# Kernel optimization log

Measured on AMD Instinct MI355X. Metric: run time of the kernel, lower is better.

## Reference

```python
import jax, jax.numpy as jnp
import numpy as np

DT = 0.01
NJ = 7
GRAV = 9.81
Q_LOWER = jnp.array([-2.9671, -1.8326, -2.9671, -3.1416, -2.9671, -0.0873, -2.9671], jnp.float32)
Q_UPPER = jnp.array([ 2.9671,  1.8326,  2.9671,  0.0,     2.9671,  3.8223,  2.9671], jnp.float32)


def _skew(v):
    z = jnp.zeros((), v.dtype)
    return jnp.stack([jnp.stack([z, -v[2], v[1]]),
                      jnp.stack([v[2], z, -v[0]]),
                      jnp.stack([-v[1], v[0], z])])


def _mot_X(E, r):
    # 6x6 spatial motion transform [[E,0],[-E*skew(r),E]]
    zero = jnp.zeros_like(E)
    top = jnp.concatenate([E, zero], axis=1)
    bot = jnp.concatenate([-E @ _skew(r), E], axis=1)
    return jnp.concatenate([top, bot], axis=0)


def _crm(v):
    # spatial motion cross-product matrix for v=[w;v0]
    Sw, Sv = _skew(v[:3]), _skew(v[3:])
    zero = jnp.zeros_like(Sw)
    top = jnp.concatenate([Sw, zero], axis=1)
    bot = jnp.concatenate([Sv, Sw], axis=1)
    return jnp.concatenate([top, bot], axis=0)


def _step_single(x, u, axes, R_tree, p_tree, I_sp):
    dt_ = x.dtype
    q = jnp.clip(x[:NJ], Q_LOWER.astype(dt_), Q_UPPER.astype(dt_))
    qd = x[NJ:]
    # forward kinematics: per-joint 6x6 child<-parent transforms and motion subspaces
    Xups, Ss = [], []
    eye3 = jnp.eye(3, dtype=dt_)
    for i in range(NJ):
        a = axes[i]
        c, s = jnp.cos(q[i]), jnp.sin(q[i])
        R = c * eye3 + s * _skew(a) + (1.0 - c) * jnp.outer(a, a)  # rodrigues
        Xj = _mot_X(R.T, jnp.zeros(3, dt_))
        Xt = _mot_X(R_tree[i], p_tree[i])
        Xups.append(Xj @ Xt)
        Ss.append(jnp.concatenate([a, jnp.zeros(3, dt_)]))
    # RNEA bias force h (qdd=0, gravity, zero base velocity, identity base pose)
    v_prev = jnp.zeros(6, dt_)
    a_prev = jnp.array([0.0, 0.0, 0.0, 0.0, 0.0, GRAV], dt_)  # a_base = -g trick
    fs = []
    for i in range(NJ):
        vJ = Ss[i] * qd[i]
        v = Xups[i] @ v_prev + vJ
        acc = Xups[i] @ a_prev + _crm(v) @ vJ
        Iv = I_sp[i] @ v
        f = I_sp[i] @ acc - _crm(v).T @ Iv  # crf(v) = -crm(v)^T
        fs.append(f)
        v_prev, a_prev = v, acc
    h = [None] * NJ
    for i in range(NJ - 1, -1, -1):
        h[i] = Ss[i] @ fs[i]
        if i > 0:
            fs[i - 1] = fs[i - 1] + Xups[i].T @ fs[i]
    h = jnp.stack(h)
    # CRBA mass matrix (serial chain, parent(i)=i-1)
    Ic = [I_sp[i] for i in range(NJ)]
    M = jnp.zeros((NJ, NJ), dt_)
    for i in range(NJ - 1, -1, -1):
        if i > 0:
            Ic[i - 1] = Ic[i - 1] + Xups[i].T @ Ic[i] @ Xups[i]
        F = Ic[i] @ Ss[i]
        M = M.at[i, i].set(Ss[i] @ F)
        for j in range(i - 1, -1, -1):
            F = Xups[j + 1].T @ F
            mij = Ss[j] @ F
            M = M.at[i, j].set(mij).at[j, i].set(mij)
    M = M + 1e-8 * jnp.eye(NJ, dtype=dt_)
    qdd = jnp.linalg.solve(M, (u - h)[:, None])[:, 0]
    qd_new = qd + DT * qdd
    q_new = q + DT * qd_new
    return jnp.concatenate([q_new, qd_new])


def setup_inputs() -> dict:
    B = 65536
    key = jax.random.key(0)
    k1, k2 = jax.random.split(key)
    x = jax.random.normal(k1, (B, 14), jnp.float32)
    u = jax.random.normal(k2, (B, 7), jnp.float32)
    rng = np.random.default_rng(0)
    # unit joint axes
    axes = rng.normal(size=(NJ, 3))
    axes = axes / np.linalg.norm(axes, axis=1, keepdims=True)
    # orthonormal fixed parent->child rotations (det +1)
    R_tree = np.empty((NJ, 3, 3))
    for i in range(NJ):
        Q, _ = np.linalg.qr(rng.normal(size=(3, 3)))
        if np.linalg.det(Q) < 0:
            Q[:, 0] = -Q[:, 0]
        R_tree[i] = Q
    p_tree = 0.2 * rng.normal(size=(NJ, 3))
    # SPD 6x6 spatial inertias: [[Ibar, m*Cx],[m*Cx^T, m*I3]]
    I_sp = np.empty((NJ, 6, 6))
    for i in range(NJ):
        m = float(rng.uniform(1.0, 5.0))
        c = 0.05 * rng.normal(size=3)
        Cx = np.array([[0, -c[2], c[1]], [c[2], 0, -c[0]], [-c[1], c[0], 0]])
        A = 0.1 * rng.normal(size=(3, 3))
        Ic_ = A @ A.T + 0.05 * np.eye(3)
        Ibar = Ic_ + m * Cx @ Cx.T
        I_sp[i] = np.block([[Ibar, m * Cx], [m * Cx.T, m * np.eye(3)]])
    return {
        "x": x, "u": u,
        "axes": jnp.asarray(axes, jnp.float32),
        "R_tree": jnp.asarray(R_tree, jnp.float32),
        "p_tree": jnp.asarray(p_tree, jnp.float32),
        "I_sp": jnp.asarray(I_sp, jnp.float32),
    }


def reference(x, u, axes, R_tree, p_tree, I_sp):
    return jax.vmap(_step_single, in_axes=(0, 0, None, None, None, None))(
        x, u, axes, R_tree, p_tree, I_sp)
```

## Files before the change

### kernel.cpp

```cpp
#include <hip/hip_runtime.h>
#include <math.h>

#define NJ 7
#define DTF 0.01f
#define GRAVF 9.81f
#define MIX(i,j) ((i)*((i)+1)/2 + (j))
#define MPAD 29

__device__ __forceinline__ void cross3(const float* a, const float* b, float* o){
    o[0] = a[1]*b[2] - a[2]*b[1];
    o[1] = a[2]*b[0] - a[0]*b[2];
    o[2] = a[0]*b[1] - a[1]*b[0];
}
__device__ __forceinline__ void mtv3(const float* E, const float* x, float* y){
    y[0] = E[0]*x[0] + E[3]*x[1] + E[6]*x[2];
    y[1] = E[1]*x[0] + E[4]*x[1] + E[7]*x[2];
    y[2] = E[2]*x[0] + E[5]*x[1] + E[8]*x[2];
}
__device__ __forceinline__ void symv(const float* S, const float* x, float* y){
    y[0] = S[0]*x[0] + S[1]*x[1] + S[2]*x[2];
    y[1] = S[1]*x[0] + S[3]*x[1] + S[4]*x[2];
    y[2] = S[2]*x[0] + S[4]*x[1] + S[5]*x[2];
}
__device__ __forceinline__ void mm3(const float* A, const float* B, float* o){
#pragma unroll
    for (int r = 0; r < 3; r++)
#pragma unroll
        for (int c = 0; c < 3; c++)
            o[r*3+c] = A[r*3]*B[c] + A[r*3+1]*B[3+c] + A[r*3+2]*B[6+c];
}
__device__ __forceinline__ void congr(const float* E, const float* X, float* o){
    float t[9];
#pragma unroll
    for (int r = 0; r < 3; r++)
#pragma unroll
        for (int c = 0; c < 3; c++)
            t[r*3+c] = E[r]*X[c] + E[3+r]*X[3+c] + E[6+r]*X[6+c];
    mm3(t, E, o);
}
__device__ __forceinline__ void makeE(const float* a, const float* __restrict__ Rt,
                                      float s, float c, float* E){
    float omc = 1.0f - c;
    float RT[9];
    RT[0] = c + omc*a[0]*a[0];       RT[1] =  s*a[2] + omc*a[0]*a[1]; RT[2] = -s*a[1] + omc*a[0]*a[2];
    RT[3] = -s*a[2] + omc*a[1]*a[0]; RT[4] = c + omc*a[1]*a[1];       RT[5] =  s*a[0] + omc*a[1]*a[2];
    RT[6] =  s*a[1] + omc*a[2]*a[0]; RT[7] = -s*a[0] + omc*a[2]*a[1]; RT[8] = c + omc*a[2]*a[2];
    float Rl[9];
#pragma unroll
    for (int k = 0; k < 9; k++) Rl[k] = Rt[k];
    mm3(RT, Rl, E);
}
__device__ __forceinline__ void bodyI(const float* __restrict__ g_I, int i,
                                      float* SA, float* h, float& m){
    const float* I6 = g_I + i*36;
    SA[0]=I6[0]; SA[1]=I6[1]; SA[2]=I6[2];
    SA[3]=I6[7]; SA[4]=I6[8]; SA[5]=I6[14];
    h[0]=I6[16]; h[1]=I6[5]; h[2]=I6[9];
    m = I6[21];
}
__device__ __forceinline__ void congrBase(const float* Ec, const float* rc,
                                          const float* SA, const float* h, float m,
                                          float* SA0, float* h0){
    float Af[9] = {SA[0],SA[1],SA[2], SA[1],SA[3],SA[4], SA[2],SA[4],SA[5]};
    float Ap[9]; congr(Ec, Af, Ap);
    float hr[3]; mtv3(Ec, h, hr);
    float hpd = hr[0]*rc[0]+hr[1]*rc[1]+hr[2]*rc[2];
    float ppd = rc[0]*rc[0]+rc[1]*rc[1]+rc[2]*rc[2];
    float dga = 2.0f*hpd + m*ppd;
    SA0[0] = Ap[0] - 2.0f*rc[0]*hr[0] - m*rc[0]*rc[0] + dga;
    SA0[1] = Ap[1] - rc[0]*hr[1] - hr[0]*rc[1] - m*rc[0]*rc[1];
    SA0[2] = Ap[2] - rc[0]*hr[2] - hr[0]*rc[2] - m*rc[0]*rc[2];
    SA0[3] = Ap[4] - 2.0f*rc[1]*hr[1] - m*rc[1]*rc[1] + dga;
    SA0[4] = Ap[5] - rc[1]*hr[2] - hr[1]*rc[2] - m*rc[1]*rc[2];
    SA0[5] = Ap[8] - 2.0f*rc[2]*hr[2] - m*rc[2]*rc[2] + dga;
    h0[0] = hr[0] + m*rc[0];
    h0[1] = hr[1] + m*rc[1];
    h0[2] = hr[2] + m*rc[2];
}

__constant__ float QL_c[NJ] = {-2.9671f,-1.8326f,-2.9671f,-3.1416f,-2.9671f,-0.0873f,-2.9671f};
__constant__ float QU_c[NJ] = { 2.9671f, 1.8326f, 2.9671f, 0.0f,    2.9671f, 3.8223f, 2.9671f};

__global__ __launch_bounds__(128)
void panda_step(const float* __restrict__ x, const float* __restrict__ u,
                const float* __restrict__ g_ax, const float* __restrict__ g_Rt,
                const float* __restrict__ g_pt, const float* __restrict__ g_I,
                float* __restrict__ out, int B)
{
    __shared__ float s_M[64*MPAD];

    const int role = threadIdx.x >> 6;
    const int lane = threadIdx.x & 63;
    const int e    = blockIdx.x*64 + lane;
    const bool act = (e < B);

    float q[NJ], qd[NJ], sn[NJ], cs[NJ];
    if (act){
        float xl[14];
        const float2* x2 = (const float2*)(x + e*14);
#pragma unroll
        for (int i = 0; i < 7; i++){ float2 v = x2[i]; xl[2*i] = v.x; xl[2*i+1] = v.y; }
#pragma unroll
        for (int i = 0; i < NJ; i++){
            q[i]  = fminf(fmaxf(xl[i], QL_c[i]), QU_c[i]);
            qd[i] = xl[NJ + i];
            __sincosf(q[i], &sn[i], &cs[i]);
        }
    }

    float rhs[NJ];

    if (act && role == 1){
        float Sw[NJ][3], Sv[NJ][3];
        float SB[NJ][6], hB[NJ][3];
        float Ec[9], rc[3];
#pragma unroll
        for (int i = 0; i < NJ; i++){
            float a[3] = { g_ax[3*i], g_ax[3*i+1], g_ax[3*i+2] };
            float p[3] = { g_pt[3*i], g_pt[3*i+1], g_pt[3*i+2] };
            float E[9]; makeE(a, g_Rt + 9*i, sn[i], cs[i], E);
            if (i == 0){
#pragma unroll
                for (int k = 0; k < 9; k++) Ec[k] = E[k];
                rc[0]=p[0]; rc[1]=p[1]; rc[2]=p[2];
            } else {
                float t3[3]; mtv3(Ec, p, t3);
                rc[0]+=t3[0]; rc[1]+=t3[1]; rc[2]+=t3[2];
                float En[9]; mm3(E, Ec, En);
#pragma unroll
                for (int k = 0; k < 9; k++) Ec[k] = En[k];
            }
            float sh[3]; mtv3(Ec, a, sh);
            float cb[3]; cross3(rc, sh, cb);
#pragma unroll
            for (int k = 0; k < 3; k++){ Sw[i][k]=sh[k]; Sv[i][k]=cb[k]; }
            float SAb[6], hb[3], mb; bodyI(g_I, i, SAb, hb, mb);
            congrBase(Ec, rc, SAb, hb, mb, &SB[i][0], &hB[i][0]);
        }
        float IcA[6] = {0,0,0,0,0,0}, Ich[3] = {0,0,0}, Icm = 0.f;
        float Mx[28];
#pragma unroll
        for (int i = NJ-1; i >= 0; i--){
#pragma unroll
            for (int k = 0; k < 6; k++) IcA[k] += SB[i][k];
#pragma unroll
            for (int k = 0; k < 3; k++) Ich[k] += hB[i][k];
            Icm += g_I[i*36 + 21];
            float Ft[3], Fb[3], t1[3], t2[3];
            symv(IcA, &Sw[i][0], Ft);
            cross3(Ich, &Sv[i][0], t1);
#pragma unroll
            for (int k = 0; k < 3; k++) Ft[k] += t1[k];
            cross3(Ich, &Sw[i][0], t2);
#pragma unroll
            for (int k = 0; k < 3; k++) Fb[k] = Icm*Sv[i][k] - t2[k];
#pragma unroll
            for (int j = 0; j < NJ; j++) if (j <= i){
                Mx[MIX(i,j)] = Sw[j][0]*Ft[0] + Sw[j][1]*Ft[1] + Sw[j][2]*Ft[2]
                             + Sv[j][0]*Fb[0] + Sv[j][1]*Fb[1] + Sv[j][2]*Fb[2];
            }
        }
#pragma unroll
        for (int i = 0; i < NJ; i++) Mx[MIX(i,i)] += 1e-8f;
#pragma unroll
        for (int k = 0; k < NJ; k++){
            float d = Mx[MIX(k,k)];
#pragma unroll
            for (int j = 0; j < NJ; j++) if (j < k) d -= Mx[MIX(k,j)]*Mx[MIX(k,j)];
            float linv = __builtin_amdgcn_rsqf(d);
            Mx[MIX(k,k)] = linv;
#pragma unroll
            for (int i2 = k+1; i2 < NJ; i2++){
                float s2 = Mx[MIX(i2,k)];
#pragma unroll
                for (int j = 0; j < NJ; j++) if (j < k) s2 -= Mx[MIX(i2,j)]*Mx[MIX(k,j)];
                Mx[MIX(i2,k)] = s2 * linv;
            }
        }
#pragma unroll
        for (int j = 0; j < 28; j++) s_M[lane*MPAD + j] = Mx[j];
    }
    else if (act){
#pragma unroll
        for (int i = 0; i < NJ; i++) rhs[i] = u[e*NJ + i];
        float Sw[NJ][3], Sv[NJ][3];
        float f0[NJ][6];
        float Ec[9], rc[3];
        float vw[3]={0,0,0}, vv[3]={0,0,0};
        float aw[3]={0,0,0}, av[3]={0,0,GRAVF};
#pragma unroll
        for (int i = 0; i < NJ; i++){
            float a[3] = { g_ax[3*i], g_ax[3*i+1], g_ax[3*i+2] };
            float p[3] = { g_pt[3*i], g_pt[3*i+1], g_pt[3*i+2] };
            float E[9]; makeE(a, g_Rt + 9*i, sn[i], cs[i], E);
            if (i == 0){
#pragma unroll
                for (int k = 0; k < 9; k++) Ec[k] = E[k];
                rc[0]=p[0]; rc[1]=p[1]; rc[2]=p[2];
            } else {
                float t3[3]; mtv3(Ec, p, t3);
                rc[0]+=t3[0]; rc[1]+=t3[1]; rc[2]+=t3[2];
                float En[9]; mm3(E, Ec, En);
#pragma unroll
                for (int k = 0; k < 9; k++) Ec[k] = En[k];
            }
            float sh[3]; mtv3(Ec, a, sh);
            float cb[3]; cross3(rc, sh, cb);
#pragma unroll
            for (int k = 0; k < 3; k++){ Sw[i][k]=sh[k]; Sv[i][k]=cb[k]; }
            float qdi = qd[i];
#pragma unroll
            for (int k = 0; k < 3; k++){ vw[k] += qdi*sh[k]; vv[k] += qdi*cb[k]; }
            float c1[3], c2[3], c3[3];
            cross3(vw, sh, c1); cross3(vw, cb, c2); cross3(vv, sh, c3);
#pragma unroll
            for (int k = 0; k < 3; k++){ aw[k] += qdi*c1[k]; av[k] += qdi*(c2[k]+c3[k]); }
            float SAb[6], hb[3], mb; bodyI(g_I, i, SAb, hb, mb);
            float SA0[6], h0[3]; congrBase(Ec, rc, SAb, hb, mb, SA0, h0);
            float Ivt[3], Ivb[3], Iat[3], Iab[3], t1[3], t2[3];
            symv(SA0, vw, Ivt); cross3(h0, vv, t1);
#pragma unroll
            for (int k = 0; k < 3; k++) Ivt[k] += t1[k];
            cross3(h0, vw, t2);
#pragma unroll
            for (int k = 0; k < 3; k++) Ivb[k] = mb*vv[k] - t2[k];
            symv(SA0, aw, Iat); cross3(h0, av, t1);
#pragma unroll
            for (int k = 0; k < 3; k++) Iat[k] += t1[k];
            cross3(h0, aw, t2);
#pragma unroll
            for (int k = 0; k < 3; k++) Iab[k] = mb*av[k] - t2[k];
            float d1[3], d2[3], d3[3];
            cross3(vw, Ivt, d1); cross3(vv, Ivb, d2); cross3(vw, Ivb, d3);
#pragma unroll
            for (int k = 0; k < 3; k++){
                f0[i][k]   = Iat[k] + d1[k] + d2[k];
                f0[i][3+k] = Iab[k] + d3[k];
            }
        }
        float g6[6] = {0,0,0,0,0,0};
#pragma unroll
        for (int i = NJ-1; i >= 0; i--){
#pragma unroll
            for (int k = 0; k < 6; k++) g6[k] += f0[i][k];
            rhs[i] -= Sw[i][0]*g6[0] + Sw[i][1]*g6[1] + Sw[i][2]*g6[2]
                    + Sv[i][0]*g6[3] + Sv[i][1]*g6[4] + Sv[i][2]*g6[5];
        }
    }

    __syncthreads();

    if (act && role == 0){
        float Mx[28];
#pragma unroll
        for (int j = 0; j < 28; j++) Mx[j] = s_M[lane*MPAD + j];
        float y[NJ];
#pragma unroll
        for (int i = 0; i < NJ; i++){
            float s2 = rhs[i];
#pragma unroll
            for (int j = 0; j < NJ; j++) if (j < i) s2 -= Mx[MIX(i,j)]*y[j];
            y[i] = s2 * Mx[MIX(i,i)];
        }
        float z[NJ];
#pragma unroll
        for (int i = NJ-1; i >= 0; i--){
            float s2 = y[i];
#pragma unroll
            for (int j = NJ-1; j >= 0; j--) if (j > i) s2 -= Mx[MIX(j,i)]*z[j];
            z[i] = s2 * Mx[MIX(i,i)];
        }
        float o14[14];
#pragma unroll
        for (int i = 0; i < NJ; i++){
            float qdn = qd[i] + DTF*z[i];
            o14[i]      = q[i] + DTF*qdn;
            o14[NJ + i] = qdn;
        }
        float2* o2 = (float2*)(out + e*14);
#pragma unroll
        for (int i = 0; i < 7; i++){ float2 v; v.x = o14[2*i]; v.y = o14[2*i+1]; o2[i] = v; }
    }
}

extern "C" void kernel_launch(void* const* d_in, const int* in_sizes, int n_in,
                              void* d_out, int out_size, void* d_ws, size_t ws_size,
                              hipStream_t stream) {
    const float* x   = (const float*)d_in[0];
    const float* u   = (const float*)d_in[1];
    const float* ax  = (const float*)d_in[2];
    const float* Rt  = (const float*)d_in[3];
    const float* pt  = (const float*)d_in[4];
    const float* Isp = (const float*)d_in[5];
    float* out = (float*)d_out;
    int B = in_sizes[0] / 14;
    int grid = (B + 63) / 64;
    hipLaunchKernelGGL(panda_step, dim3(grid), dim3(128), 0, stream,
                       x, u, ax, Rt, pt, Isp, out, B);
}
```

Before: 83.84 us.

## Compute RNEA bias forces in local body frames instead of base frame

```diff
diff --git a/kernel.cpp b/kernel.cpp
--- a/kernel.cpp
+++ b/kernel.cpp
@@ -11,6 +11,11 @@
     o[0] = a[1]*b[2] - a[2]*b[1];
     o[1] = a[2]*b[0] - a[0]*b[2];
     o[2] = a[0]*b[1] - a[1]*b[0];
+}
+__device__ __forceinline__ void mv3(const float* E, const float* x, float* y){
+    y[0] = E[0]*x[0] + E[1]*x[1] + E[2]*x[2];
+    y[1] = E[3]*x[0] + E[4]*x[1] + E[5]*x[2];
+    y[2] = E[6]*x[0] + E[7]*x[1] + E[8]*x[2];
 }
 __device__ __forceinline__ void mtv3(const float* E, const float* x, float* y){
     y[0] = E[0]*x[0] + E[3]*x[1] + E[6]*x[2];
@@ -183,68 +188,64 @@
     else if (act){
 #pragma unroll
         for (int i = 0; i < NJ; i++) rhs[i] = u[e*NJ + i];
-        float Sw[NJ][3], Sv[NJ][3];
-        float f0[NJ][6];
-        float Ec[9], rc[3];
-        float vw[3]={0,0,0}, vv[3]={0,0,0};
-        float aw[3]={0,0,0}, av[3]={0,0,GRAVF};
+        float Earr[NJ][9];
+        float FF[NJ][6];
+        float w[3]  = {0.f,0.f,0.f}, vl[3] = {0.f,0.f,0.f};
+        float aw[3] = {0.f,0.f,0.f}, av[3] = {0.f,0.f,GRAVF};
 #pragma unroll
         for (int i = 0; i < NJ; i++){
             float a[3] = { g_ax[3*i], g_ax[3*i+1], g_ax[3*i+2] };
             float p[3] = { g_pt[3*i], g_pt[3*i+1], g_pt[3*i+2] };
-            float E[9]; makeE(a, g_Rt + 9*i, sn[i], cs[i], E);
-            if (i == 0){
-#pragma unroll
-                for (int k = 0; k < 9; k++) Ec[k] = E[k];
-                rc[0]=p[0]; rc[1]=p[1]; rc[2]=p[2];
-            } else {
-                float t3[3]; mtv3(Ec, p, t3);
-                rc[0]+=t3[0]; rc[1]+=t3[1]; rc[2]+=t3[2];
-                float En[9]; mm3(E, Ec, En);
-#pragma unroll
-                for (int k = 0; k < 9; k++) Ec[k] = En[k];
+            float* E = &Earr[i][0];
+            makeE(a, g_Rt + 9*i, sn[i], cs[i], E);
+            float qdi = qd[i];
+            float tw[3]; mv3(E, w, tw);
+            float nw[3] = { tw[0]+a[0]*qdi, tw[1]+a[1]*qdi, tw[2]+a[2]*qdi };
+            float cwp[3]; cross3(w, p, cwp);
+            float t1[3] = { vl[0]+cwp[0], vl[1]+cwp[1], vl[2]+cwp[2] };
+            float nvl[3]; mv3(E, t1, nvl);
+            float taw[3]; mv3(E, aw, taw);
+            float cna[3]; cross3(nw, a, cna);
+            float naw[3] = { taw[0]+qdi*cna[0], taw[1]+qdi*cna[1], taw[2]+qdi*cna[2] };
+            float cap[3]; cross3(aw, p, cap);
+            float t2[3] = { av[0]+cap[0], av[1]+cap[1], av[2]+cap[2] };
+            float tav[3]; mv3(E, t2, tav);
+            float cva[3]; cross3(nvl, a, cva);
+            float nav[3] = { tav[0]+qdi*cva[0], tav[1]+qdi*cva[1], tav[2]+qdi*cva[2] };
+            float SAi[6], hi[3], mi; bodyI(g_I, i, SAi, hi, mi);
+            float Ivt[3], Iat[3], hxv[3], hxa[3];
+            symv(SAi, nw, Ivt);  cross3(hi, nvl, hxv);
+            symv(SAi, naw, Iat); cross3(hi, nav, hxa);
+#pragma unroll
+            for (int k = 0; k < 3; k++){ Ivt[k] += hxv[k]; Iat[k] += hxa[k]; }
+            float hxw[3], hxaw[3];
+            cross3(hi, nw, hxw); cross3(hi, naw, hxaw);
+            float Ivb[3] = { mi*nvl[0]-hxw[0], mi*nvl[1]-hxw[1], mi*nvl[2]-hxw[2] };
+            float Iab[3] = { mi*nav[0]-hxaw[0], mi*nav[1]-hxaw[1], mi*nav[2]-hxaw[2] };
+            float c1[3], c2[3], c3[3];
+            cross3(nw, Ivt, c1); cross3(nvl, Ivb, c2); cross3(nw, Ivb, c3);
+            FF[i][0] = Iat[0]+c1[0]+c2[0];
+            FF[i][1] = Iat[1]+c1[1]+c2[1];
+            FF[i][2] = Iat[2]+c1[2]+c2[2];
+            FF[i][3] = Iab[0]+c3[0];
+            FF[i][4] = Iab[1]+c3[1];
+            FF[i][5] = Iab[2]+c3[2];
+#pragma unroll
+            for (int k = 0; k < 3; k++){ w[k]=nw[k]; vl[k]=nvl[k]; aw[k]=naw[k]; av[k]=nav[k]; }
+        }
+#pragma unroll
+        for (int i = NJ-1; i >= 0; i--){
+            float a[3] = { g_ax[3*i], g_ax[3*i+1], g_ax[3*i+2] };
+            rhs[i] -= a[0]*FF[i][0] + a[1]*FF[i][1] + a[2]*FF[i][2];
+            if (i > 0){
+                float p[3] = { g_pt[3*i], g_pt[3*i+1], g_pt[3*i+2] };
+                const float* E = &Earr[i][0];
+                float tm[3], tf[3], cp[3];
+                mtv3(E, &FF[i][0], tm); mtv3(E, &FF[i][3], tf);
+                cross3(p, tf, cp);
+                FF[i-1][0]+=tm[0]+cp[0]; FF[i-1][1]+=tm[1]+cp[1]; FF[i-1][2]+=tm[2]+cp[2];
+                FF[i-1][3]+=tf[0];       FF[i-1][4]+=tf[1];       FF[i-1][5]+=tf[2];
             }
-            float sh[3]; mtv3(Ec, a, sh);
-            float cb[3]; cross3(rc, sh, cb);
-#pragma unroll
-            for (int k = 0; k < 3; k++){ Sw[i][k]=sh[k]; Sv[i][k]=cb[k]; }
-            float qdi = qd[i];
-#pragma unroll
-            for (int k = 0; k < 3; k++){ vw[k] += qdi*sh[k]; vv[k] += qdi*cb[k]; }
-            float c1[3], c2[3], c3[3];
-            cross3(vw, sh, c1); cross3(vw, cb, c2); cross3(vv, sh, c3);
-#pragma unroll
-            for (int k = 0; k < 3; k++){ aw[k] += qdi*c1[k]; av[k] += qdi*(c2[k]+c3[k]); }
-            float SAb[6], hb[3], mb; bodyI(g_I, i, SAb, hb, mb);
-            float SA0[6], h0[3]; congrBase(Ec, rc, SAb, hb, mb, SA0, h0);
-            float Ivt[3], Ivb[3], Iat[3], Iab[3], t1[3], t2[3];
-            symv(SA0, vw, Ivt); cross3(h0, vv, t1);
-#pragma unroll
-            for (int k = 0; k < 3; k++) Ivt[k] += t1[k];
-            cross3(h0, vw, t2);
-#pragma unroll
-            for (int k = 0; k < 3; k++) Ivb[k] = mb*vv[k] - t2[k];
-            symv(SA0, aw, Iat); cross3(h0, av, t1);
-#pragma unroll
-            for (int k = 0; k < 3; k++) Iat[k] += t1[k];
-            cross3(h0, aw, t2);
-#pragma unroll
-            for (int k = 0; k < 3; k++) Iab[k] = mb*av[k] - t2[k];
-            float d1[3], d2[3], d3[3];
-            cross3(vw, Ivt, d1); cross3(vv, Ivb, d2); cross3(vw, Ivb, d3);
-#pragma unroll
-            for (int k = 0; k < 3; k++){
-                f0[i][k]   = Iat[k] + d1[k] + d2[k];
-                f0[i][3+k] = Iab[k] + d3[k];
-            }
-        }
-        float g6[6] = {0,0,0,0,0,0};
-#pragma unroll
-        for (int i = NJ-1; i >= 0; i--){
-#pragma unroll
-            for (int k = 0; k < 6; k++) g6[k] += f0[i][k];
-            rhs[i] -= Sw[i][0]*g6[0] + Sw[i][1]*g6[1] + Sw[i][2]*g6[2]
-                    + Sv[i][0]*g6[3] + Sv[i][1]*g6[4] + Sv[i][2]*g6[5];
         }
     }
 
```

Measured after the change: 77.72 us. 7.3% less time.
